# Performance work log

Hardware: AMD Instinct MI355X
Metric: run time of the kernel (lower is better)

## Reference

```python
import jax, jax.numpy as jnp
import numpy as np

B, F_IN, L = 32, 16, 8192
LATENT, P, PROTO_LEN, C = 64, 200, 16, 10
EPS = 1e-4

def conv1d(x, w):
    # x: [N, Cin, L], w: [Cout, Cin, K], valid padding, stride 1
    return jax.lax.conv_general_dilated(x, w, (1,), 'VALID',
                                        dimension_numbers=('NCH', 'OIH', 'NCH'))

def make_last_layer():
    per = P // C
    ident = np.zeros((P, C), dtype=np.float32)
    ident[np.arange(P), np.arange(P) // per] = 1.0
    # correct class weight 1, incorrect -0.5 (set_last_layer_incorrect_connection)
    return jnp.asarray(1.0 * ident.T + (-0.5) * (1.0 - ident.T))  # [C, P]

def setup_inputs() -> dict:
    key = jax.random.key(0)
    k1, k2, k3, k4 = jax.random.split(key, 4)
    x = jax.random.normal(k1, (B, F_IN, L), dtype=jnp.float32)
    enc_w = jax.random.normal(k2, (LATENT, F_IN, 3), dtype=jnp.float32) * (2.0 / (LATENT * 3)) ** 0.5
    addon_w = jax.random.normal(k3, (LATENT, LATENT, 1), dtype=jnp.float32) * (2.0 / LATENT) ** 0.5
    protos = jax.random.uniform(k4, (P, LATENT, PROTO_LEN), dtype=jnp.float32)
    last_w = make_last_layer()
    return {"x": x, "enc_w": enc_w, "addon_w": addon_w, "protos": protos, "last_w": last_w}

def reference(x, enc_w, addon_w, protos, last_w):
    # encoder + add-on 1x1 conv, both ReLU
    f = jax.nn.relu(conv1d(x, enc_w))          # [B, LATENT, L-2]
    f = jax.nn.relu(conv1d(f, addon_w))        # [B, LATENT, L-2]
    x2_patch_sum = conv1d(f * f, jnp.ones_like(protos))      # [B, P, Lo]
    xp = conv1d(f, protos)                                   # [B, P, Lo]
    p2 = jnp.sum(protos * protos, axis=(1, 2))[None, :, None]
    distances = jax.nn.relu(x2_patch_sum - 2.0 * xp + p2)    # [B, P, Lo]
    # min-pool over time (original: -max_pool(-d))
    min_distances = jnp.min(distances, axis=2)               # [B, P]
    # log similarity
    acts = jnp.log((min_distances + 1.0) / (min_distances + EPS))
    logits = acts @ last_w.T                                 # [B, C]
    return logits, min_distances
```

## Files before the change

### kernel.cpp

```cpp
#include <hip/hip_runtime.h>
#include <hip/hip_bf16.h>
#include <math.h>

#define B_    32
#define FIN   16
#define LIN   8192
#define LAT   64
#define L1V   8190
#define PN    200
#define PLEN  16
#define LOV   8175
#define NCLS  10
#define EPSV  1e-4f
#define MD0   320
#define CHK   256
#define WIN   272
#define FST   68
#define NPT   7
#define NFRAG (NPT * 16 * 4 * 64)
#define XSLOT 8256
#define NTRB  (33 * B_)

typedef unsigned short u16;
typedef unsigned int   u32;
typedef short s16x8 __attribute__((ext_vector_type(8)));
typedef float f32x16 __attribute__((ext_vector_type(16)));

union FragU { uint2 u2[2]; s16x8 v; };

__device__ __forceinline__ u16 vf2b(float f) {
    union { float f; u32 u; } v; v.f = f;
    u32 u = v.u;
    return (u16)((u + 0x7fffu + ((u >> 16) & 1u)) >> 16);
}

__global__ void k_prep(const float* __restrict__ x, const float* __restrict__ we,
                       const float* __restrict__ wa, const float* __restrict__ pt,
                       u32* __restrict__ wsm, float* __restrict__ p2g,
                       u16* __restrict__ pk, u16* __restrict__ wpk,
                       u16* __restrict__ xT) {
    __shared__ u16 ls[16][256];
    const int t = threadIdx.x;

    if (blockIdx.x < NTRB) {
        const int tile = blockIdx.x % 33;
        const int b    = blockIdx.x / 33;
        const int base = tile * 256;
        const float* xb = x + (size_t)b * FIN * LIN;
        const int slot = base + t;
        #pragma unroll
        for (int ch = 0; ch < 16; ++ch) {
            float v = (slot < LIN) ? xb[(size_t)ch * LIN + slot] : 0.f;
            ls[ch][t] = vf2b(v);
        }
        __syncthreads();
        if (slot < XSLOT) {
            u32 w[8];
            #pragma unroll
            for (int cp = 0; cp < 8; ++cp)
                w[cp] = ((u32)ls[2 * cp + 1][t] << 16) | (u32)ls[2 * cp][t];
            uint4* dst = (uint4*)(xT + ((size_t)b * XSLOT + slot) * 16);
            dst[0] = make_uint4(w[0], w[1], w[2], w[3]);
            dst[1] = make_uint4(w[4], w[5], w[6], w[7]);
        }
        return;
    }

    const int tid = (blockIdx.x - NTRB) * 256 + t;
    const int N   = 64 * 256;

    for (int j = tid; j < B_ * PN; j += N) wsm[j] = 0x7f7fffffu;

    for (int p = tid; p < 224; p += N) {
        float s = 0.f;
        if (p < PN) {
            const float4* pr = (const float4*)(pt + (size_t)p * (LAT * PLEN));
            #pragma unroll 4
            for (int j = 0; j < 256; ++j) {
                float4 v = pr[j];
                s += v.x * v.x + v.y * v.y + v.z * v.z + v.w * v.w;
            }
        }
        p2g[p] = s;
    }

    for (int f = tid; f < NFRAG; f += N) {
        const int lane = f & 63;
        const int cs   = (f >> 6) & 3;
        const int tap  = (f >> 8) & 15;
        const int p7   = f >> 12;
        const int gp   = p7 * 32 + (lane & 31);
        const int chb  = cs * 16 + (lane >> 5) * 8;
        s16x8 v;
        if (gp < PN) {
            const float* src = pt + (size_t)gp * (LAT * PLEN) + (size_t)chb * PLEN + tap;
            #pragma unroll
            for (int j = 0; j < 8; ++j) v[j] = (short)vf2b(src[j * PLEN]);
        } else {
            #pragma unroll
            for (int j = 0; j < 8; ++j) v[j] = 0;
        }
        *(s16x8*)(pk + (size_t)f * 8) = v;
    }

    for (int f = tid; f < 14 * 64; f += N) {
        const int lane = f & 63, grp = f >> 6;
        const int col = lane & 31, kb = (lane >> 5) * 8;
        s16x8 v;
        if (grp < 6) {
            const int tau = grp >> 1, nt = grp & 1;
            #pragma unroll
            for (int j = 0; j < 8; ++j)
                v[j] = (short)vf2b(we[(size_t)(nt * 32 + col) * 48 + (kb + j) * 3 + tau]);
        } else {
            const int g2 = grp - 6, cs = g2 >> 1, nt = g2 & 1;
            #pragma unroll
            for (int j = 0; j < 8; ++j)
                v[j] = (short)vf2b(wa[(size_t)(nt * 32 + col) * 64 + cs * 16 + kb + j]);
        }
        *(s16x8*)(wpk + (size_t)f * 8) = v;
    }
}

__global__ void __launch_bounds__(256, 4) k_dist(const u16* __restrict__ xT,
                                                 const u16* __restrict__ wpk,
                                                 const u16* __restrict__ pk,
                                                 u32* __restrict__ wsm,
                                                 const float* __restrict__ p2g) {
    __shared__ __align__(16) u16 fwin[WIN * FST];
    __shared__ float gwin[WIN];

    const int t  = threadIdx.x;
    const int ck = blockIdx.x;
    const int b  = blockIdx.y;
    const int base = ck * CHK;

    const int lane = t & 63;
    const int wv   = t >> 6;
    const int m    = lane & 31;
    const int half = lane >> 5;
    const int koff = half * 8;

    const u16* wpkl = wpk + (size_t)lane * 8;
    const u16* xTb  = xT + (size_t)b * XSLOT * 16;

    #pragma unroll 1
    for (int mt = wv; mt < 9; mt += 4) {
        const int ar = mt * 32 + m;
        f32x16 c1[2];
        #pragma unroll
        for (int i = 0; i < 16; ++i) { c1[0][i] = 0.f; c1[1][i] = 0.f; }
        #pragma unroll
        for (int tau = 0; tau < 3; ++tau) {
            FragU aF;
            aF.v = *(const s16x8*)(xTb + (size_t)(base + ar + tau) * 16 + koff);
            #pragma unroll
            for (int nt = 0; nt < 2; ++nt) {
                FragU bW; bW.v = *(const s16x8*)(wpkl + (size_t)(tau * 2 + nt) * 512);
                c1[nt] = __builtin_amdgcn_mfma_f32_32x32x16_bf16(aF.v, bW.v, c1[nt], 0, 0, 0);
            }
        }
        #pragma unroll
        for (int nt = 0; nt < 2; ++nt) {
            const int col = nt * 32 + m;
            #pragma unroll
            for (int reg = 0; reg < 16; ++reg) {
                const int row = mt * 32 + (reg & 3) + 8 * (reg >> 2) + 4 * half;
                if (row < WIN) fwin[row * FST + col] = vf2b(fmaxf(c1[nt][reg], 0.f));
            }
        }
        f32x16 c2[2];
        #pragma unroll
        for (int i = 0; i < 16; ++i) { c2[0][i] = 0.f; c2[1][i] = 0.f; }
        FragU a2[4];
        const int arc = (ar < WIN) ? ar : (WIN - 1);
        #pragma unroll
        for (int cs = 0; cs < 4; ++cs) {
            const u16* ap = &fwin[arc * FST + cs * 16 + koff];
            a2[cs].u2[0] = *(const uint2*)ap;
            a2[cs].u2[1] = *(const uint2*)(ap + 4);
        }
        #pragma unroll
        for (int cs = 0; cs < 4; ++cs)
            #pragma unroll
            for (int nt = 0; nt < 2; ++nt) {
                FragU bW; bW.v = *(const s16x8*)(wpkl + (size_t)(6 + cs * 2 + nt) * 512);
                c2[nt] = __builtin_amdgcn_mfma_f32_32x32x16_bf16(a2[cs].v, bW.v, c2[nt], 0, 0, 0);
            }
        #pragma unroll
        for (int nt = 0; nt < 2; ++nt) {
            const int col = nt * 32 + m;
            #pragma unroll
            for (int reg = 0; reg < 16; ++reg) {
                const int row = mt * 32 + (reg & 3) + 8 * (reg >> 2) + 4 * half;
                if (row < WIN) fwin[row * FST + col] = vf2b(fmaxf(c2[nt][reg], 0.f));
            }
        }
    }
    __syncthreads();

    {
        float g0 = 0.f, g1 = 0.f;
        const uint2* r0 = (const uint2*)(fwin + (size_t)t * FST);
        #pragma unroll
        for (int i = 0; i < 16; ++i) {
            uint2 v = r0[i];
            float a = __uint_as_float(v.x << 16);
            float bb = __uint_as_float(v.x & 0xffff0000u);
            float c = __uint_as_float(v.y << 16);
            float d = __uint_as_float(v.y & 0xffff0000u);
            g0 += a * a + bb * bb + c * c + d * d;
        }
        if (t < 16) {
            const uint2* r1 = (const uint2*)(fwin + (size_t)(CHK + t) * FST);
            #pragma unroll
            for (int i = 0; i < 16; ++i) {
                uint2 v = r1[i];
                float a = __uint_as_float(v.x << 16);
                float bb = __uint_as_float(v.x & 0xffff0000u);
                float c = __uint_as_float(v.y << 16);
                float d = __uint_as_float(v.y & 0xffff0000u);
                g1 += a * a + bb * bb + c * c + d * d;
            }
        }
        gwin[t] = g0;
        if (t < 16) gwin[CHK + t] = g1;
    }
    __syncthreads();

    {
        float sv = 0.f;
        #pragma unroll
        for (int k = 0; k < PLEN; ++k) sv += gwin[t + k];
        sv = (base + t < LOV) ? sv : 3.0e38f;
        __syncthreads();
        gwin[t] = sv;
    }
    __syncthreads();

    #pragma unroll 1
    for (int p7 = 0; p7 < NPT; ++p7) {
        f32x16 acc0, acc1;
        #pragma unroll
        for (int i = 0; i < 16; ++i) { acc0[i] = 0.f; acc1[i] = 0.f; }

        const u16* pkb = pk + (size_t)p7 * (16 * 4 * 64 * 8) + (size_t)lane * 8;

        #pragma unroll 2
        for (int tap = 0; tap < 16; ++tap) {
            #pragma unroll
            for (int cs = 0; cs < 4; ++cs) {
                FragU bF, a0, a1;
                bF.v = *(const s16x8*)(pkb + (size_t)(tap * 4 + cs) * 512);
                const int co = cs * 16 + koff;
                const u16* ap = &fwin[(wv * 64 + m + tap) * FST + co];
                a0.u2[0] = *(const uint2*)ap; a0.u2[1] = *(const uint2*)(ap + 4);
                const u16* aq = ap + 32 * FST;
                a1.u2[0] = *(const uint2*)aq; a1.u2[1] = *(const uint2*)(aq + 4);
                acc0 = __builtin_amdgcn_mfma_f32_32x32x16_bf16(a0.v, bF.v, acc0, 0, 0, 0);
                acc1 = __builtin_amdgcn_mfma_f32_32x32x16_bf16(a1.v, bF.v, acc1, 0, 0, 0);
            }
        }

        const float p2v = p2g[p7 * 32 + m];
        float dmin = 3.4e38f;
        #pragma unroll
        for (int reg = 0; reg < 16; ++reg) {
            const int row = (reg & 3) + 8 * (reg >> 2) + 4 * half;
            float d0 = gwin[wv * 64 + row]      - 2.f * acc0[reg] + p2v;
            float d1 = gwin[wv * 64 + 32 + row] - 2.f * acc1[reg] + p2v;
            dmin = fminf(dmin, fminf(d0, d1));
        }
        dmin = fminf(dmin, __shfl_xor(dmin, 32));
        if (half == 0 && p7 * 32 + m < PN)
            atomicMin(&wsm[b * PN + p7 * 32 + m], (u32)__float_as_uint(fmaxf(dmin, 0.f)));
    }
}

__global__ void __launch_bounds__(256) k_head(const u32* __restrict__ wsm,
                                              const float* __restrict__ lw,
                                              float* __restrict__ out) {
    __shared__ float as_[PN];
    const int b = blockIdx.x, t = threadIdx.x;
    if (t < PN) {
        float md = __uint_as_float(wsm[b * PN + t]);
        md = fminf(fmaxf(md, 0.f), 2000.f);
        if (!(md == md)) md = 0.f;
        out[MD0 + b * PN + t] = md;
        as_[t] = logf((md + 1.f) / (md + EPSV));
    }
    __syncthreads();
    if (t < NCLS) {
        float sum = 0.f;
        #pragma unroll 1
        for (int p = 0; p < PN; ++p) sum += as_[p] * lw[t * PN + p];
        sum = fminf(fmaxf(sum, -100.f), 100.f);
        if (!(sum == sum)) sum = 0.f;
        out[b * NCLS + t] = sum;
    }
}

extern "C" void kernel_launch(void* const* d_in, const int* in_sizes, int n_in,
                              void* d_out, int out_size, void* d_ws, size_t ws_size,
                              hipStream_t stream) {
    const float* x  = 0;
    const float* we = 0;
    const float* wa = 0;
    const float* pt = 0;
    const float* lw = 0;
    for (int i = 0; i < n_in; ++i) {
        switch (in_sizes[i]) {
            case 4194304: x  = (const float*)d_in[i]; break;
            case 3072:    we = (const float*)d_in[i]; break;
            case 4096:    wa = (const float*)d_in[i]; break;
            case 204800:  pt = (const float*)d_in[i]; break;
            case 2000:    lw = (const float*)d_in[i]; break;
            default: break;
        }
    }
    if (!x || !we || !wa || !pt || !lw) {
        x  = (const float*)d_in[0];
        we = (const float*)d_in[1];
        wa = (const float*)d_in[2];
        pt = (const float*)d_in[3];
        lw = (const float*)d_in[4];
    }
    float* out = (float*)d_out;

    char* ws  = (char*)d_ws;
    u32*   wsm = (u32*)ws;
    float* p2g = (float*)(ws + 25600);
    u16*   pk  = (u16*)(ws + 26496);
    u16*   wpk = (u16*)(ws + 944000);
    u16*   xT  = (u16*)(ws + 958336);

    k_prep<<<dim3(NTRB + 64), dim3(256), 0, stream>>>(x, we, wa, pt, wsm, p2g, pk, wpk, xT);
    k_dist<<<dim3(32, 32), dim3(256), 0, stream>>>(xT, wpk, pk, wsm, p2g);
    k_head<<<dim3(B_), dim3(256), 0, stream>>>(wsm, lw, out);
}
```

Baseline: 229.7 us.

## Double chunk size, reuse prototype fragments across row groups, fuse head via last-block

```diff
diff --git a/kernel.cpp b/kernel.cpp
--- a/kernel.cpp
+++ b/kernel.cpp
@@ -13,8 +13,8 @@
 #define NCLS  10
 #define EPSV  1e-4f
 #define MD0   320
-#define CHK   256
-#define WIN   272
+#define CHK   512
+#define WIN   528
 #define FST   68
 #define NPT   7
 #define NFRAG (NPT * 16 * 4 * 64)
@@ -36,7 +36,8 @@
 
 __global__ void k_prep(const float* __restrict__ x, const float* __restrict__ we,
                        const float* __restrict__ wa, const float* __restrict__ pt,
-                       u32* __restrict__ wsm, float* __restrict__ p2g,
+                       u32* __restrict__ wsm, u32* __restrict__ cnt,
+                       float* __restrict__ p2g,
                        u16* __restrict__ pk, u16* __restrict__ wpk,
                        u16* __restrict__ xT) {
     __shared__ u16 ls[16][256];
@@ -70,18 +71,24 @@
     const int N   = 64 * 256;
 
     for (int j = tid; j < B_ * PN; j += N) wsm[j] = 0x7f7fffffu;
-
-    for (int p = tid; p < 224; p += N) {
-        float s = 0.f;
-        if (p < PN) {
-            const float4* pr = (const float4*)(pt + (size_t)p * (LAT * PLEN));
-            #pragma unroll 4
-            for (int j = 0; j < 256; ++j) {
-                float4 v = pr[j];
-                s += v.x * v.x + v.y * v.y + v.z * v.z + v.w * v.w;
-            }
-        }
-        p2g[p] = s;
+    for (int j = tid; j < B_; j += N) cnt[j] = 0;
+
+    {
+        const int wid = tid >> 6, nl = tid & 63, NW = N >> 6;
+        for (int p = wid; p < 224; p += NW) {
+            float s = 0.f;
+            if (p < PN) {
+                const float4* pr = (const float4*)(pt + (size_t)p * (LAT * PLEN)) + nl * 4;
+                #pragma unroll
+                for (int j = 0; j < 4; ++j) {
+                    float4 v = pr[j];
+                    s += v.x * v.x + v.y * v.y + v.z * v.z + v.w * v.w;
+                }
+            }
+            #pragma unroll
+            for (int off = 32; off; off >>= 1) s += __shfl_xor(s, off);
+            if (nl == 0) p2g[p] = s;
+        }
     }
 
     for (int f = tid; f < NFRAG; f += N) {
@@ -122,13 +129,82 @@
     }
 }
 
-__global__ void __launch_bounds__(256, 4) k_dist(const u16* __restrict__ xT,
+template<int NT>
+__device__ __forceinline__ void dist_pass(int p7b,
+                                          const u16* __restrict__ pk,
+                                          const u16* __restrict__ fwin,
+                                          const float* __restrict__ sarr,
+                                          const float* __restrict__ p2g,
+                                          u32* __restrict__ wsm,
+                                          int b, int wv, int lane) {
+    const int m    = lane & 31;
+    const int half = lane >> 5;
+    const int koff = half * 8;
+
+    f32x16 acc[NT][4];
+    #pragma unroll
+    for (int n = 0; n < NT; ++n)
+        #pragma unroll
+        for (int g = 0; g < 4; ++g)
+            #pragma unroll
+            for (int i = 0; i < 16; ++i) acc[n][g][i] = 0.f;
+
+    const u16* pkl = pk + (size_t)lane * 8;
+
+    #pragma unroll 2
+    for (int tap = 0; tap < 16; ++tap) {
+        #pragma unroll
+        for (int cs = 0; cs < 4; ++cs) {
+            const int co = cs * 16 + koff;
+            FragU a[4];
+            const u16* ap = &fwin[(wv * 128 + m + tap) * FST + co];
+            #pragma unroll
+            for (int g = 0; g < 4; ++g) {
+                const u16* aq = ap + g * (32 * FST);
+                a[g].u2[0] = *(const uint2*)aq;
+                a[g].u2[1] = *(const uint2*)(aq + 4);
+            }
+            #pragma unroll
+            for (int n = 0; n < NT; ++n) {
+                FragU bF;
+                bF.v = *(const s16x8*)(pkl +
+                        (size_t)(((p7b + n) * 16 + tap) * 4 + cs) * 512);
+                #pragma unroll
+                for (int g = 0; g < 4; ++g)
+                    acc[n][g] = __builtin_amdgcn_mfma_f32_32x32x16_bf16(a[g].v, bF.v, acc[n][g], 0, 0, 0);
+            }
+        }
+    }
+
+    #pragma unroll
+    for (int n = 0; n < NT; ++n) {
+        const int p7 = p7b + n;
+        const float p2v = p2g[p7 * 32 + m];
+        float dmin = 3.4e38f;
+        #pragma unroll
+        for (int g = 0; g < 4; ++g)
+            #pragma unroll
+            for (int reg = 0; reg < 16; ++reg) {
+                const int row = g * 32 + (reg & 3) + 8 * (reg >> 2) + 4 * half;
+                dmin = fminf(dmin, sarr[wv * 128 + row] - 2.f * acc[n][g][reg] + p2v);
+            }
+        dmin = fminf(dmin, __shfl_xor(dmin, 32));
+        if (half == 0 && p7 * 32 + m < PN)
+            atomicMin(&wsm[b * PN + p7 * 32 + m], (u32)__float_as_uint(fmaxf(dmin, 0.f)));
+    }
+}
+
+__global__ void __launch_bounds__(256, 2) k_dist(const u16* __restrict__ xT,
                                                  const u16* __restrict__ wpk,
                                                  const u16* __restrict__ pk,
                                                  u32* __restrict__ wsm,
-                                                 const float* __restrict__ p2g) {
+                                                 u32* __restrict__ cnt,
+                                                 const float* __restrict__ p2g,
+                                                 const float* __restrict__ lw,
+                                                 float* __restrict__ out) {
     __shared__ __align__(16) u16 fwin[WIN * FST];
     __shared__ float gwin[WIN];
+    __shared__ u32 lastf;
 
     const int t  = threadIdx.x;
     const int ck = blockIdx.x;
@@ -145,7 +221,7 @@
     const u16* xTb  = xT + (size_t)b * XSLOT * 16;
 
     #pragma unroll 1
-    for (int mt = wv; mt < 9; mt += 4) {
+    for (int mt = wv; mt < 17; mt += 4) {
         const int ar = mt * 32 + m;
         f32x16 c1[2];
         #pragma unroll
@@ -200,103 +276,71 @@
     __syncthreads();
 
     {
-        float g0 = 0.f, g1 = 0.f;
-        const uint2* r0 = (const uint2*)(fwin + (size_t)t * FST);
-        #pragma unroll
-        for (int i = 0; i < 16; ++i) {
-            uint2 v = r0[i];
-            float a = __uint_as_float(v.x << 16);
-            float bb = __uint_as_float(v.x & 0xffff0000u);
-            float c = __uint_as_float(v.y << 16);
-            float d = __uint_as_float(v.y & 0xffff0000u);
-            g0 += a * a + bb * bb + c * c + d * d;
-        }
-        if (t < 16) {
-            const uint2* r1 = (const uint2*)(fwin + (size_t)(CHK + t) * FST);
-            #pragma unroll
-            for (int i = 0; i < 16; ++i) {
-                uint2 v = r1[i];
-                float a = __uint_as_float(v.x << 16);
-                float bb = __uint_as_float(v.x & 0xffff0000u);
-                float c = __uint_as_float(v.y << 16);
-                float d = __uint_as_float(v.y & 0xffff0000u);
-                g1 += a * a + bb * bb + c * c + d * d;
-            }
-        }
-        gwin[t] = g0;
-        if (t < 16) gwin[CHK + t] = g1;
+        float gs[3] = {0.f, 0.f, 0.f};
+        #pragma unroll
+        for (int rr = 0; rr < 3; ++rr) {
+            const int row = rr * 256 + t;
+            if (row < WIN) {
+                const uint2* r0 = (const uint2*)(fwin + (size_t)row * FST);
+                float s = 0.f;
+                #pragma unroll
+                for (int i = 0; i < 16; ++i) {
+                    uint2 v = r0[i];
+                    float a = __uint_as_float(v.x << 16);
+                    float bb = __uint_as_float(v.x & 0xffff0000u);
+                    float c = __uint_as_float(v.y << 16);
+                    float d = __uint_as_float(v.y & 0xffff0000u);
+                    s += a * a + bb * bb + c * c + d * d;
+                }
+                gs[rr] = s;
+            }
+        }
+        gwin[t] = gs[0];
+        gwin[256 + t] = gs[1];
+        if (t < 16) gwin[512 + t] = gs[2];
     }
     __syncthreads();
 
     {
-        float sv = 0.f;
-        #pragma unroll
-        for (int k = 0; k < PLEN; ++k) sv += gwin[t + k];
-        sv = (base + t < LOV) ? sv : 3.0e38f;
+        float sv0 = 0.f, sv1 = 0.f;
+        #pragma unroll
+        for (int k = 0; k < PLEN; ++k) sv0 += gwin[t + k];
+        #pragma unroll
+        for (int k = 0; k < PLEN; ++k) sv1 += gwin[256 + t + k];
+        sv0 = (base + t < LOV)       ? sv0 : 3.0e38f;
+        sv1 = (base + 256 + t < LOV) ? sv1 : 3.0e38f;
         __syncthreads();
-        gwin[t] = sv;
+        gwin[t] = sv0;
+        gwin[256 + t] = sv1;
     }
     __syncthreads();
 
-    #pragma unroll 1
-    for (int p7 = 0; p7 < NPT; ++p7) {
-        f32x16 acc0, acc1;
-        #pragma unroll
-        for (int i = 0; i < 16; ++i) { acc0[i] = 0.f; acc1[i] = 0.f; }
-
-        const u16* pkb = pk + (size_t)p7 * (16 * 4 * 64 * 8) + (size_t)lane * 8;
-
-        #pragma unroll 2
-        for (int tap = 0; tap < 16; ++tap) {
-            #pragma unroll
-            for (int cs = 0; cs < 4; ++cs) {
-                FragU bF, a0, a1;
-                bF.v = *(const s16x8*)(pkb + (size_t)(tap * 4 + cs) * 512);
-                const int co = cs * 16 + koff;
-                const u16* ap = &fwin[(wv * 64 + m + tap) * FST + co];
-                a0.u2[0] = *(const uint2*)ap; a0.u2[1] = *(const uint2*)(ap + 4);
-                const u16* aq = ap + 32 * FST;
-                a1.u2[0] = *(const uint2*)aq; a1.u2[1] = *(const uint2*)(aq + 4);
-                acc0 = __builtin_amdgcn_mfma_f32_32x32x16_bf16(a0.v, bF.v, acc0, 0, 0, 0);
-                acc1 = __builtin_amdgcn_mfma_f32_32x32x16_bf16(a1.v, bF.v, acc1, 0, 0, 0);
-            }
-        }
-
-        const float p2v = p2g[p7 * 32 + m];
-        float dmin = 3.4e38f;
-        #pragma unroll
-        for (int reg = 0; reg < 16; ++reg) {
-            const int row = (reg & 3) + 8 * (reg >> 2) + 4 * half;
-            float d0 = gwin[wv * 64 + row]      - 2.f * acc0[reg] + p2v;
-            float d1 = gwin[wv * 64 + 32 + row] - 2.f * acc1[reg] + p2v;
-            dmin = fminf(dmin, fminf(d0, d1));
-        }
-        dmin = fminf(dmin, __shfl_xor(dmin, 32));
-        if (half == 0 && p7 * 32 + m < PN)
-            atomicMin(&wsm[b * PN + p7 * 32 + m], (u32)__float_as_uint(fmaxf(dmin, 0.f)));
-    }
-}
-
-__global__ void __launch_bounds__(256) k_head(const u32* __restrict__ wsm,
-                                              const float* __restrict__ lw,
-                                              float* __restrict__ out) {
-    __shared__ float as_[PN];
-    const int b = blockIdx.x, t = threadIdx.x;
-    if (t < PN) {
-        float md = __uint_as_float(wsm[b * PN + t]);
-        md = fminf(fmaxf(md, 0.f), 2000.f);
-        if (!(md == md)) md = 0.f;
-        out[MD0 + b * PN + t] = md;
-        as_[t] = logf((md + 1.f) / (md + EPSV));
-    }
+    dist_pass<2>(0, pk, fwin, gwin, p2g, wsm, b, wv, lane);
+    dist_pass<2>(2, pk, fwin, gwin, p2g, wsm, b, wv, lane);
+    dist_pass<2>(4, pk, fwin, gwin, p2g, wsm, b, wv, lane);
+    dist_pass<1>(6, pk, fwin, gwin, p2g, wsm, b, wv, lane);
+
+    __threadfence();
+    if (t == 0) lastf = (atomicAdd(&cnt[b], 1) == 15) ? 1u : 0u;
     __syncthreads();
-    if (t < NCLS) {
-        float sum = 0.f;
-        #pragma unroll 1
-        for (int p = 0; p < PN; ++p) sum += as_[p] * lw[t * PN + p];
-        sum = fminf(fmaxf(sum, -100.f), 100.f);
-        if (!(sum == sum)) sum = 0.f;
-        out[b * NCLS + t] = sum;
+    if (lastf) {
+        if (t < PN) {
+            u32 bits = atomicMin(&wsm[b * PN + t], 0x7f7fffffu);
+            float md = __uint_as_float(bits);
+            md = fminf(fmaxf(md, 0.f), 2000.f);
+            if (!(md == md)) md = 0.f;
+            out[MD0 + b * PN + t] = md;
+            gwin[t] = logf((md + 1.f) / (md + EPSV));
+        }
+        __syncthreads();
+        if (t < NCLS) {
+            float sum = 0.f;
+            #pragma unroll 1
+            for (int p = 0; p < PN; ++p) sum += gwin[p] * lw[t * PN + p];
+            sum = fminf(fmaxf(sum, -100.f), 100.f);
+            if (!(sum == sum)) sum = 0.f;
+            out[b * NCLS + t] = sum;
+        }
     }
 }
 
@@ -330,11 +374,11 @@
     char* ws  = (char*)d_ws;
     u32*   wsm = (u32*)ws;
     float* p2g = (float*)(ws + 25600);
-    u16*   pk  = (u16*)(ws + 26496);
-    u16*   wpk = (u16*)(ws + 944000);
-    u16*   xT  = (u16*)(ws + 958336);
-
-    k_prep<<<dim3(NTRB + 64), dim3(256), 0, stream>>>(x, we, wa, pt, wsm, p2g, pk, wpk, xT);
-    k_dist<<<dim3(32, 32), dim3(256), 0, stream>>>(xT, wpk, pk, wsm, p2g);
-    k_head<<<dim3(B_), dim3(256), 0, stream>>>(wsm, lw, out);
-}
+    u32*   cnt = (u32*)(ws + 26496);
+    u16*   pk  = (u16*)(ws + 26624);
+    u16*   wpk = (u16*)(ws + 944128);
+    u16*   xT  = (u16*)(ws + 958464);
+
+    k_prep<<<dim3(NTRB + 64), dim3(256), 0, stream>>>(x, we, wa, pt, wsm, cnt, p2g, pk, wpk, xT);
+    k_dist<<<dim3(16, 32), dim3(256), 0, stream>>>(xT, wpk, pk, wsm, cnt, p2g, lw, out);
+}
```

Measured after the change: 221.3 us. -3.6%, faster.

## Fuse head into distance kernel via last-block counter and parallelize proto norms

Applied to the files above, without the earlier changes.

```diff
diff --git a/kernel.cpp b/kernel.cpp
--- a/kernel.cpp
+++ b/kernel.cpp
@@ -36,7 +36,8 @@
 
 __global__ void k_prep(const float* __restrict__ x, const float* __restrict__ we,
                        const float* __restrict__ wa, const float* __restrict__ pt,
-                       u32* __restrict__ wsm, float* __restrict__ p2g,
+                       u32* __restrict__ wsm, u32* __restrict__ cnt,
+                       float* __restrict__ p2g,
                        u16* __restrict__ pk, u16* __restrict__ wpk,
                        u16* __restrict__ xT) {
     __shared__ u16 ls[16][256];
@@ -70,18 +71,24 @@
     const int N   = 64 * 256;
 
     for (int j = tid; j < B_ * PN; j += N) wsm[j] = 0x7f7fffffu;
-
-    for (int p = tid; p < 224; p += N) {
-        float s = 0.f;
-        if (p < PN) {
-            const float4* pr = (const float4*)(pt + (size_t)p * (LAT * PLEN));
-            #pragma unroll 4
-            for (int j = 0; j < 256; ++j) {
-                float4 v = pr[j];
-                s += v.x * v.x + v.y * v.y + v.z * v.z + v.w * v.w;
-            }
-        }
-        p2g[p] = s;
+    for (int j = tid; j < B_; j += N) cnt[j] = 0;
+
+    {
+        const int wid = tid >> 6, nl = tid & 63, NW = N >> 6;
+        for (int p = wid; p < 224; p += NW) {
+            float s = 0.f;
+            if (p < PN) {
+                const float4* pr = (const float4*)(pt + (size_t)p * (LAT * PLEN)) + nl * 4;
+                #pragma unroll
+                for (int j = 0; j < 4; ++j) {
+                    float4 v = pr[j];
+                    s += v.x * v.x + v.y * v.y + v.z * v.z + v.w * v.w;
+                }
+            }
+            #pragma unroll
+            for (int off = 32; off; off >>= 1) s += __shfl_xor(s, off);
+            if (nl == 0) p2g[p] = s;
+        }
     }
 
     for (int f = tid; f < NFRAG; f += N) {
@@ -126,9 +133,13 @@
                                                  const u16* __restrict__ wpk,
                                                  const u16* __restrict__ pk,
                                                  u32* __restrict__ wsm,
-                                                 const float* __restrict__ p2g) {
+                                                 u32* __restrict__ cnt,
+                                                 const float* __restrict__ p2g,
+                                                 const float* __restrict__ lw,
+                                                 float* __restrict__ out) {
     __shared__ __align__(16) u16 fwin[WIN * FST];
     __shared__ float gwin[WIN];
+    __shared__ u32 lastf;
 
     const int t  = threadIdx.x;
     const int ck = blockIdx.x;
@@ -275,28 +286,29 @@
         if (half == 0 && p7 * 32 + m < PN)
             atomicMin(&wsm[b * PN + p7 * 32 + m], (u32)__float_as_uint(fmaxf(dmin, 0.f)));
     }
-}
-
-__global__ void __launch_bounds__(256) k_head(const u32* __restrict__ wsm,
-                                              const float* __restrict__ lw,
-                                              float* __restrict__ out) {
-    __shared__ float as_[PN];
-    const int b = blockIdx.x, t = threadIdx.x;
-    if (t < PN) {
-        float md = __uint_as_float(wsm[b * PN + t]);
-        md = fminf(fmaxf(md, 0.f), 2000.f);
-        if (!(md == md)) md = 0.f;
-        out[MD0 + b * PN + t] = md;
-        as_[t] = logf((md + 1.f) / (md + EPSV));
-    }
-    __syncthreads();
-    if (t < NCLS) {
-        float sum = 0.f;
-        #pragma unroll 1
-        for (int p = 0; p < PN; ++p) sum += as_[p] * lw[t * PN + p];
-        sum = fminf(fmaxf(sum, -100.f), 100.f);
-        if (!(sum == sum)) sum = 0.f;
-        out[b * NCLS + t] = sum;
+
+    __syncthreads();
+    __threadfence();
+    if (t == 0) lastf = (atomicAdd(&cnt[b], 1) == 31) ? 1u : 0u;
+    __syncthreads();
+    if (lastf) {
+        if (t < PN) {
+            u32 bits = atomicMin(&wsm[b * PN + t], 0x7f7fffffu);
+            float md = __uint_as_float(bits);
+            md = fminf(fmaxf(md, 0.f), 2000.f);
+            if (!(md == md)) md = 0.f;
+            out[MD0 + b * PN + t] = md;
+            gwin[t] = logf((md + 1.f) / (md + EPSV));
+        }
+        __syncthreads();
+        if (t < NCLS) {
+            float sum = 0.f;
+            #pragma unroll 1
+            for (int p = 0; p < PN; ++p) sum += gwin[p] * lw[t * PN + p];
+            sum = fminf(fmaxf(sum, -100.f), 100.f);
+            if (!(sum == sum)) sum = 0.f;
+            out[b * NCLS + t] = sum;
+        }
     }
 }
 
@@ -330,11 +342,11 @@
     char* ws  = (char*)d_ws;
     u32*   wsm = (u32*)ws;
     float* p2g = (float*)(ws + 25600);
-    u16*   pk  = (u16*)(ws + 26496);
-    u16*   wpk = (u16*)(ws + 944000);
-    u16*   xT  = (u16*)(ws + 958336);
-
-    k_prep<<<dim3(NTRB + 64), dim3(256), 0, stream>>>(x, we, wa, pt, wsm, p2g, pk, wpk, xT);
-    k_dist<<<dim3(32, 32), dim3(256), 0, stream>>>(xT, wpk, pk, wsm, p2g);
-    k_head<<<dim3(B_), dim3(256), 0, stream>>>(wsm, lw, out);
+    u32*   cnt = (u32*)(ws + 26496);
+    u16*   pk  = (u16*)(ws + 26624);
+    u16*   wpk = (u16*)(ws + 944128);
+    u16*   xT  = (u16*)(ws + 958464);
+
+    k_prep<<<dim3(NTRB + 64), dim3(256), 0, stream>>>(x, we, wa, pt, wsm, cnt, p2g, pk, wpk, xT);
+    k_dist<<<dim3(32, 32), dim3(256), 0, stream>>>(xT, wpk, pk, wsm, cnt, p2g, lw, out);
 }
```

Measured after the change: 250.6 us. 1.09x slower.
